# Kernel tuning notes

Hardware: AMD Instinct MI355X
Metric: run time of the kernel (lower is better)

Reference implementation:

```python
import jax, jax.numpy as jnp
import numpy as np


def _cdist(x, y):
    # x: (b, n, c), y: (b, m, c) -> (b, n, m) Euclidean distances
    x2 = jnp.sum(x * x, axis=-1, keepdims=True)          # (b, n, 1)
    y2 = jnp.sum(y * y, axis=-1)[:, None, :]             # (b, 1, m)
    xy = jnp.einsum('bnc,bmc->bnm', x, y)                # (b, n, m)
    d2 = jnp.maximum(x2 + y2 - 2.0 * xy, 0.0)
    return jnp.sqrt(d2)


def setup_inputs() -> dict:
    key = jax.random.key(0)
    k1, k2, k3, k4 = jax.random.split(key, 4)
    bs, N, M, C = 8, 4096, 4096, 128
    return {
        'set1': jax.random.normal(k1, (bs, N, C), dtype=jnp.float32),
        'set2': jax.random.normal(k2, (bs, M, C), dtype=jnp.float32),
        'w1': jax.random.uniform(k3, (bs, N), dtype=jnp.float32),
        'w2': jax.random.uniform(k4, (bs, M), dtype=jnp.float32),
    }


def reference(set1, set2, w1, w2):
    dist = _cdist(set1, set2)                 # (b, N, M)
    out_dist = jnp.min(dist, axis=2)          # (b, N)
    out_dist2 = jnp.min(dist, axis=1)         # (b, M)
    total = (jnp.sum(w1 * out_dist) + jnp.sum(w2 * out_dist2)) / 2.0
    return total
```

## Files before the change

### kernel.cpp

```cpp
#include <hip/hip_runtime.h>

#define BS 8
#define NN 4096
#define MM 4096
#define CC 128
#define XT 128
#define MT 128
#define MH 2048
#define NMT (MH / MT)
#define NXT (NN / XT)

#define FINF_BITS 0x7F800000u

typedef __attribute__((ext_vector_type(8))) short bf16x8;
typedef __attribute__((ext_vector_type(4))) float f32x4;

__device__ inline ushort f2bf(float f) {
    unsigned u = __float_as_uint(f);
    unsigned r = (u + 0x7FFFu + ((u >> 16) & 1u)) >> 16;
    return (ushort)r;
}

__global__ void ch_prep(const float* __restrict__ x, const float* __restrict__ y,
                        ushort* __restrict__ x16, ushort* __restrict__ y16,
                        float* __restrict__ xn, float* __restrict__ yn,
                        unsigned* __restrict__ rowmin, unsigned* __restrict__ colmin,
                        float* __restrict__ out) {
    int gid = blockIdx.x * blockDim.x + threadIdx.x;
    size_t i = (size_t)gid * 4;

    float4 v = *(const float4*)(x + i);
    ushort4 o;
    o.x = f2bf(v.x); o.y = f2bf(v.y); o.z = f2bf(v.z); o.w = f2bf(v.w);
    *(ushort4*)(x16 + i) = o;
    float sx = v.x * v.x + v.y * v.y + v.z * v.z + v.w * v.w;

    float4 w = *(const float4*)(y + i);
    ushort4 p;
    p.x = f2bf(w.x); p.y = f2bf(w.y); p.z = f2bf(w.z); p.w = f2bf(w.w);
    *(ushort4*)(y16 + i) = p;
    float sy = w.x * w.x + w.y * w.y + w.z * w.z + w.w * w.w;

#pragma unroll
    for (int mask = 1; mask <= 16; mask <<= 1) {
        sx += __shfl_xor(sx, mask, 64);
        sy += __shfl_xor(sy, mask, 64);
    }
    if ((threadIdx.x & 31) == 0) {
        int row = gid >> 5;
        xn[row] = sx;
        yn[row] = sy;
    }
    if (gid < BS * NN) {
        rowmin[gid] = FINF_BITS;
        colmin[gid] = FINF_BITS;
    }
    if (gid == 0) out[0] = 0.0f;
}

__global__ __launch_bounds__(512) void ch_tile(
    const ushort* __restrict__ X, const ushort* __restrict__ Y,
    const float* __restrict__ xn, const float* __restrict__ yn,
    unsigned* __restrict__ rowmin, unsigned* __restrict__ colmin) {

    __shared__ ushort xs[XT * CC];
    __shared__ unsigned coltile[MH];
    __shared__ unsigned rowtile[XT];

    const int b  = blockIdx.z;
    const int xt = blockIdx.x;
    const int mh = blockIdx.y;
    const int n0 = xt * XT;
    const int m0 = mh * MH;
    const int tid  = threadIdx.x;
    const int wave = tid >> 6;
    const int lane = tid & 63;
    const int lc   = lane & 15;
    const int quad = lane >> 4;
    const int wm = wave >> 2;
    const int wn = wave & 3;

    const ushort* Xb = X + ((size_t)b * NN + n0) * CC;
#pragma unroll
    for (int s = 0; s < 4; ++s) {
        int flat = s * 512 + tid;
        int r = flat >> 4, c = flat & 15;
        int cs = c ^ (r & 7);
        *(bf16x8*)(xs + r * CC + cs * 8) = *(const bf16x8*)(Xb + (size_t)r * CC + c * 8);
    }
    for (int c2 = tid; c2 < MH; c2 += 512) coltile[c2] = FINF_BITS;
    if (tid < XT) rowtile[tid] = FINF_BITS;
    __syncthreads();

    float rm[4][4];
#pragma unroll
    for (int i = 0; i < 4; ++i)
#pragma unroll
        for (int r = 0; r < 4; ++r) rm[i][r] = __builtin_inff();

    const ushort* Yb  = Y + ((size_t)b * MM + m0) * CC;
    const float*  ynb = yn + (size_t)b * MM + m0;
    const float*  xnb = xn + (size_t)b * NN + n0;
    const int xrow = (wm * 64 + lc) * CC;
    const int xsw  = lc & 7;

#pragma unroll 1
    for (int mt = 0; mt < NMT; ++mt) {
        const ushort* Ymt = Yb + (size_t)(mt * MT + wn * 32 + lc) * CC + quad * 8;

        float ynr[2];
#pragma unroll
        for (int j = 0; j < 2; ++j)
            ynr[j] = ynb[mt * MT + wn * 32 + j * 16 + lc];

        f32x4 acc[4][2];
        const f32x4 z = {0.f, 0.f, 0.f, 0.f};
#pragma unroll
        for (int kt = 0; kt < 4; ++kt) {
            bf16x8 af[4], yf[2];
            const int cs = ((kt * 4 + quad) ^ xsw) * 8;
#pragma unroll
            for (int j = 0; j < 2; ++j)
                yf[j] = *(const bf16x8*)(Ymt + (size_t)j * 16 * CC + kt * 32);
#pragma unroll
            for (int i = 0; i < 4; ++i)
                af[i] = *(const bf16x8*)(xs + xrow + i * 16 * CC + cs);
#pragma unroll
            for (int j = 0; j < 2; ++j)
#pragma unroll
                for (int i = 0; i < 4; ++i)
                    acc[i][j] = __builtin_amdgcn_mfma_f32_16x16x32_bf16(
                        af[i], yf[j], (kt == 0) ? z : acc[i][j], 0, 0, 0);
        }

        float cmv[2];
#pragma unroll
        for (int j = 0; j < 2; ++j) cmv[j] = __builtin_inff();

#pragma unroll
        for (int i = 0; i < 4; ++i) {
            float4 t = *(const float4*)(xnb + wm * 64 + i * 16 + quad * 4);
            float xnr[4] = {t.x, t.y, t.z, t.w};
#pragma unroll
            for (int j = 0; j < 2; ++j) {
                f32x4 a = acc[i][j];
#pragma unroll
                for (int r = 0; r < 4; ++r) {
                    float d2 = xnr[r] + fmaf(-2.0f, a[r], ynr[j]);
                    rm[i][r] = fminf(rm[i][r], d2);
                    cmv[j]   = fminf(cmv[j], d2);
                }
            }
        }

#pragma unroll
        for (int mask = 16; mask <= 32; mask <<= 1)
#pragma unroll
            for (int j = 0; j < 2; ++j)
                cmv[j] = fminf(cmv[j], __shfl_xor(cmv[j], mask, 64));
        if (quad == 0) {
#pragma unroll
            for (int j = 0; j < 2; ++j)
                atomicMin(&coltile[mt * MT + wn * 32 + j * 16 + lc],
                          __float_as_uint(fmaxf(cmv[j], 0.0f)));
        }
    }

#pragma unroll
    for (int mask = 1; mask <= 8; mask <<= 1)
#pragma unroll
        for (int i = 0; i < 4; ++i)
#pragma unroll
            for (int r = 0; r < 4; ++r)
                rm[i][r] = fminf(rm[i][r], __shfl_xor(rm[i][r], mask, 64));
    if (lc == 0) {
#pragma unroll
        for (int i = 0; i < 4; ++i)
#pragma unroll
            for (int r = 0; r < 4; ++r)
                atomicMin(&rowtile[wm * 64 + i * 16 + quad * 4 + r],
                          __float_as_uint(fmaxf(rm[i][r], 0.0f)));
    }

    __syncthreads();
    if (tid < XT)
        atomicMin(&rowmin[(size_t)b * NN + n0 + tid], rowtile[tid]);
    for (int c2 = tid; c2 < MH; c2 += 512)
        atomicMin(&colmin[(size_t)b * MM + m0 + c2], coltile[c2]);
}

__global__ void ch_finalize(const unsigned* __restrict__ rowmin,
                            const unsigned* __restrict__ colmin,
                            const float* __restrict__ w1,
                            const float* __restrict__ w2,
                            float* __restrict__ out) {
    int i = blockIdx.x * blockDim.x + threadIdx.x;
    int stride = gridDim.x * blockDim.x;
    float s = 0.f;
    for (int idx = i; idx < BS * NN; idx += stride)
        s += w1[idx] * sqrtf(__uint_as_float(rowmin[idx])) +
             w2[idx] * sqrtf(__uint_as_float(colmin[idx]));
#pragma unroll
    for (int off = 32; off > 0; off >>= 1) s += __shfl_down(s, off, 64);
    __shared__ float ls[4];
    int lane = threadIdx.x & 63, wv = threadIdx.x >> 6;
    if (lane == 0) ls[wv] = s;
    __syncthreads();
    if (threadIdx.x == 0) {
        float t = ls[0] + ls[1] + ls[2] + ls[3];
        atomicAdd(out, 0.5f * t);
    }
}

extern "C" void kernel_launch(void* const* d_in, const int* in_sizes, int n_in,
                              void* d_out, int out_size, void* d_ws, size_t ws_size,
                              hipStream_t stream) {
    const float* set1 = (const float*)d_in[0];
    const float* set2 = (const float*)d_in[1];
    const float* w1   = (const float*)d_in[2];
    const float* w2   = (const float*)d_in[3];
    float* out = (float*)d_out;

    ushort*   x16    = (ushort*)d_ws;
    ushort*   y16    = x16 + (size_t)BS * NN * CC;
    float*    xn     = (float*)(y16 + (size_t)BS * MM * CC);
    float*    yn     = xn + BS * NN;
    unsigned* rowmin = (unsigned*)(yn + BS * MM);
    unsigned* colmin = rowmin + BS * NN;

    ch_prep<<<BS * NN * CC / 4 / 256, 256, 0, stream>>>(
        set1, set2, x16, y16, xn, yn, rowmin, colmin, out);

    dim3 grid(NXT, MM / MH, BS);
    ch_tile<<<grid, 512, 0, stream>>>(x16, y16, xn, yn, rowmin, colmin);

    ch_finalize<<<64, 256, 0, stream>>>(rowmin, colmin, w1, w2, out);
}
```

Before: 154.9 us.

## Give each block full M range, register double-buffer Y, atomics straight to global colmin

Each block now owns a 128-row X tile and sweeps all of M, so row minima are written directly without global atomics. Each wave takes a 16-column Y strip against all 128 X rows (8 MFMA accumulators), with the X norms held in registers. Y fragments are double-buffered in registers across M tiles to hide global load latency. Column minima go through global atomicMin directly rather than a shared-memory column tile. The grid shrinks to 256 blocks (bs-major order), which may reduce occupancy and adds contention on the global column atomics.

```diff
diff --git a/kernel.cpp b/kernel.cpp
--- a/kernel.cpp
+++ b/kernel.cpp
@@ -6,8 +6,7 @@
 #define CC 128
 #define XT 128
 #define MT 128
-#define MH 2048
-#define NMT (MH / MT)
+#define NMT (MM / MT)
 #define NXT (NN / XT)
 
 #define FINF_BITS 0x7F800000u
@@ -24,8 +23,7 @@
 __global__ void ch_prep(const float* __restrict__ x, const float* __restrict__ y,
                         ushort* __restrict__ x16, ushort* __restrict__ y16,
                         float* __restrict__ xn, float* __restrict__ yn,
-                        unsigned* __restrict__ rowmin, unsigned* __restrict__ colmin,
-                        float* __restrict__ out) {
+                        unsigned* __restrict__ colmin, float* __restrict__ out) {
     int gid = blockIdx.x * blockDim.x + threadIdx.x;
     size_t i = (size_t)gid * 4;
 
@@ -51,34 +49,27 @@
         xn[row] = sx;
         yn[row] = sy;
     }
-    if (gid < BS * NN) {
-        rowmin[gid] = FINF_BITS;
-        colmin[gid] = FINF_BITS;
-    }
+    if (gid < BS * MM) colmin[gid] = FINF_BITS;
     if (gid == 0) out[0] = 0.0f;
 }
 
 __global__ __launch_bounds__(512) void ch_tile(
     const ushort* __restrict__ X, const ushort* __restrict__ Y,
     const float* __restrict__ xn, const float* __restrict__ yn,
-    unsigned* __restrict__ rowmin, unsigned* __restrict__ colmin) {
+    float* __restrict__ rowmin, unsigned* __restrict__ colmin) {
 
     __shared__ ushort xs[XT * CC];
-    __shared__ unsigned coltile[MH];
     __shared__ unsigned rowtile[XT];
 
-    const int b  = blockIdx.z;
-    const int xt = blockIdx.x;
-    const int mh = blockIdx.y;
+    const int b  = blockIdx.x;
+    const int xt = blockIdx.y;
     const int n0 = xt * XT;
-    const int m0 = mh * MH;
     const int tid  = threadIdx.x;
     const int wave = tid >> 6;
     const int lane = tid & 63;
     const int lc   = lane & 15;
     const int quad = lane >> 4;
-    const int wm = wave >> 2;
-    const int wn = wave & 3;
+    const int ycol = wave * 16 + lc;
 
     const ushort* Xb = X + ((size_t)b * NN + n0) * CC;
 #pragma unroll
@@ -88,108 +79,96 @@
         int cs = c ^ (r & 7);
         *(bf16x8*)(xs + r * CC + cs * 8) = *(const bf16x8*)(Xb + (size_t)r * CC + c * 8);
     }
-    for (int c2 = tid; c2 < MH; c2 += 512) coltile[c2] = FINF_BITS;
     if (tid < XT) rowtile[tid] = FINF_BITS;
     __syncthreads();
 
-    float rm[4][4];
-#pragma unroll
-    for (int i = 0; i < 4; ++i)
+    float xnr[8][4];
+#pragma unroll
+    for (int i = 0; i < 8; ++i) {
+        float4 t = *(const float4*)(xn + (size_t)b * NN + n0 + i * 16 + quad * 4);
+        xnr[i][0] = t.x; xnr[i][1] = t.y; xnr[i][2] = t.z; xnr[i][3] = t.w;
+    }
+    float rm[8][4];
+#pragma unroll
+    for (int i = 0; i < 8; ++i)
 #pragma unroll
         for (int r = 0; r < 4; ++r) rm[i][r] = __builtin_inff();
 
-    const ushort* Yb  = Y + ((size_t)b * MM + m0) * CC;
-    const float*  ynb = yn + (size_t)b * MM + m0;
-    const float*  xnb = xn + (size_t)b * NN + n0;
-    const int xrow = (wm * 64 + lc) * CC;
-    const int xsw  = lc & 7;
-
-#pragma unroll 1
-    for (int mt = 0; mt < NMT; ++mt) {
-        const ushort* Ymt = Yb + (size_t)(mt * MT + wn * 32 + lc) * CC + quad * 8;
-
-        float ynr[2];
-#pragma unroll
-        for (int j = 0; j < 2; ++j)
-            ynr[j] = ynb[mt * MT + wn * 32 + j * 16 + lc];
-
-        f32x4 acc[4][2];
+    const ushort* Yb  = Y + (size_t)b * MM * CC;
+    const float*  ynb = yn + (size_t)b * MM;
+    const int xsw = lc & 7;
+
+    auto loady = [&](int mt, bf16x8* yf, float& ynr) {
+        const ushort* yp = Yb + (size_t)(mt * MT + ycol) * CC + quad * 8;
+#pragma unroll
+        for (int kt = 0; kt < 4; ++kt)
+            yf[kt] = *(const bf16x8*)(yp + kt * 32);
+        ynr = ynb[mt * MT + ycol];
+    };
+
+    auto compute = [&](int mt, const bf16x8* yf, float ynr) {
+        f32x4 acc[8];
         const f32x4 z = {0.f, 0.f, 0.f, 0.f};
 #pragma unroll
         for (int kt = 0; kt < 4; ++kt) {
-            bf16x8 af[4], yf[2];
             const int cs = ((kt * 4 + quad) ^ xsw) * 8;
 #pragma unroll
-            for (int j = 0; j < 2; ++j)
-                yf[j] = *(const bf16x8*)(Ymt + (size_t)j * 16 * CC + kt * 32);
-#pragma unroll
-            for (int i = 0; i < 4; ++i)
-                af[i] = *(const bf16x8*)(xs + xrow + i * 16 * CC + cs);
-#pragma unroll
-            for (int j = 0; j < 2; ++j)
-#pragma unroll
-                for (int i = 0; i < 4; ++i)
-                    acc[i][j] = __builtin_amdgcn_mfma_f32_16x16x32_bf16(
-                        af[i], yf[j], (kt == 0) ? z : acc[i][j], 0, 0, 0);
-        }
-
-        float cmv[2];
-#pragma unroll
-        for (int j = 0; j < 2; ++j) cmv[j] = __builtin_inff();
-
-#pragma unroll
-        for (int i = 0; i < 4; ++i) {
-            float4 t = *(const float4*)(xnb + wm * 64 + i * 16 + quad * 4);
-            float xnr[4] = {t.x, t.y, t.z, t.w};
-#pragma unroll
-            for (int j = 0; j < 2; ++j) {
-                f32x4 a = acc[i][j];
-#pragma unroll
-                for (int r = 0; r < 4; ++r) {
-                    float d2 = xnr[r] + fmaf(-2.0f, a[r], ynr[j]);
-                    rm[i][r] = fminf(rm[i][r], d2);
-                    cmv[j]   = fminf(cmv[j], d2);
-                }
+            for (int i = 0; i < 8; ++i) {
+                bf16x8 af = *(const bf16x8*)(xs + (i * 16 + lc) * CC + cs);
+                acc[i] = __builtin_amdgcn_mfma_f32_16x16x32_bf16(
+                    af, yf[kt], (kt == 0) ? z : acc[i], 0, 0, 0);
             }
         }
-
-#pragma unroll
-        for (int mask = 16; mask <= 32; mask <<= 1)
-#pragma unroll
-            for (int j = 0; j < 2; ++j)
-                cmv[j] = fminf(cmv[j], __shfl_xor(cmv[j], mask, 64));
-        if (quad == 0) {
-#pragma unroll
-            for (int j = 0; j < 2; ++j)
-                atomicMin(&coltile[mt * MT + wn * 32 + j * 16 + lc],
-                          __float_as_uint(fmaxf(cmv[j], 0.0f)));
+        float cmv = __builtin_inff();
+#pragma unroll
+        for (int i = 0; i < 8; ++i) {
+            f32x4 a = acc[i];
+#pragma unroll
+            for (int r = 0; r < 4; ++r) {
+                float d2 = xnr[i][r] + fmaf(-2.0f, a[r], ynr);
+                rm[i][r] = fminf(rm[i][r], d2);
+                cmv      = fminf(cmv, d2);
+            }
         }
+        cmv = fminf(cmv, __shfl_xor(cmv, 16, 64));
+        cmv = fminf(cmv, __shfl_xor(cmv, 32, 64));
+        if (quad == 0)
+            atomicMin(&colmin[(size_t)b * MM + mt * MT + ycol],
+                      __float_as_uint(fmaxf(cmv, 0.0f)));
+    };
+
+    bf16x8 yfA[4], yfB[4];
+    float ynrA, ynrB;
+    loady(0, yfA, ynrA);
+#pragma unroll 1
+    for (int mt = 0; mt < NMT; mt += 2) {
+        loady(mt + 1, yfB, ynrB);
+        compute(mt, yfA, ynrA);
+        loady((mt + 2 < NMT) ? mt + 2 : 0, yfA, ynrA);
+        compute(mt + 1, yfB, ynrB);
     }
 
 #pragma unroll
     for (int mask = 1; mask <= 8; mask <<= 1)
 #pragma unroll
-        for (int i = 0; i < 4; ++i)
+        for (int i = 0; i < 8; ++i)
 #pragma unroll
             for (int r = 0; r < 4; ++r)
                 rm[i][r] = fminf(rm[i][r], __shfl_xor(rm[i][r], mask, 64));
     if (lc == 0) {
 #pragma unroll
-        for (int i = 0; i < 4; ++i)
+        for (int i = 0; i < 8; ++i)
 #pragma unroll
             for (int r = 0; r < 4; ++r)
-                atomicMin(&rowtile[wm * 64 + i * 16 + quad * 4 + r],
+                atomicMin(&rowtile[i * 16 + quad * 4 + r],
                           __float_as_uint(fmaxf(rm[i][r], 0.0f)));
     }
-
     __syncthreads();
     if (tid < XT)
-        atomicMin(&rowmin[(size_t)b * NN + n0 + tid], rowtile[tid]);
-    for (int c2 = tid; c2 < MH; c2 += 512)
-        atomicMin(&colmin[(size_t)b * MM + m0 + c2], coltile[c2]);
-}
-
-__global__ void ch_finalize(const unsigned* __restrict__ rowmin,
+        rowmin[(size_t)b * NN + n0 + tid] = __uint_as_float(rowtile[tid]);
+}
+
+__global__ void ch_finalize(const float* __restrict__ rowmin,
                             const unsigned* __restrict__ colmin,
                             const float* __restrict__ w1,
                             const float* __restrict__ w2,
@@ -198,7 +177,7 @@
     int stride = gridDim.x * blockDim.x;
     float s = 0.f;
     for (int idx = i; idx < BS * NN; idx += stride)
-        s += w1[idx] * sqrtf(__uint_as_float(rowmin[idx])) +
+        s += w1[idx] * sqrtf(rowmin[idx]) +
              w2[idx] * sqrtf(__uint_as_float(colmin[idx]));
 #pragma unroll
     for (int off = 32; off > 0; off >>= 1) s += __shfl_down(s, off, 64);
@@ -225,13 +204,13 @@
     ushort*   y16    = x16 + (size_t)BS * NN * CC;
     float*    xn     = (float*)(y16 + (size_t)BS * MM * CC);
     float*    yn     = xn + BS * NN;
-    unsigned* rowmin = (unsigned*)(yn + BS * MM);
-    unsigned* colmin = rowmin + BS * NN;
+    float*    rowmin = yn + BS * MM;
+    unsigned* colmin = (unsigned*)(rowmin + BS * NN);
 
     ch_prep<<<BS * NN * CC / 4 / 256, 256, 0, stream>>>(
-        set1, set2, x16, y16, xn, yn, rowmin, colmin, out);
-
-    dim3 grid(NXT, MM / MH, BS);
+        set1, set2, x16, y16, xn, yn, colmin, out);
+
+    dim3 grid(BS, NXT);
     ch_tile<<<grid, 512, 0, stream>>>(x16, y16, xn, yn, rowmin, colmin);
 
     ch_finalize<<<64, 256, 0, stream>>>(rowmin, colmin, w1, w2, out);
```

Result: slower. 224.4 us (+44.9%).

## Fuse X conversion into tile kernel and fold finalize via last-block reduction

Applied to the files above, without the earlier changes.

The X-side bf16 conversion and row norms move out of the prep kernel and into the tile kernel, which now reads fp32 X directly, converts it while staging into shared memory, and computes the norms there. The separate finalize kernel is removed: a global done counter lets the last tile block do the weighted reduction and write the output. This drops one launch and a round trip through global memory for X16/xn. In exchange, the fp32 X tile is read twice across the M halves, each block does extra conversion work, and a threadfence plus atomic is added per block.

```diff
diff --git a/kernel.cpp b/kernel.cpp
--- a/kernel.cpp
+++ b/kernel.cpp
@@ -9,6 +9,7 @@
 #define MH 2048
 #define NMT (MH / MT)
 #define NXT (NN / XT)
+#define NBLK (NXT * (MM / MH) * BS)
 
 #define FINF_BITS 0x7F800000u
 
@@ -21,19 +22,12 @@
     return (ushort)r;
 }
 
-__global__ void ch_prep(const float* __restrict__ x, const float* __restrict__ y,
-                        ushort* __restrict__ x16, ushort* __restrict__ y16,
-                        float* __restrict__ xn, float* __restrict__ yn,
+__global__ void ch_prep(const float* __restrict__ y,
+                        ushort* __restrict__ y16, float* __restrict__ yn,
                         unsigned* __restrict__ rowmin, unsigned* __restrict__ colmin,
-                        float* __restrict__ out) {
+                        unsigned* __restrict__ done, float* __restrict__ out) {
     int gid = blockIdx.x * blockDim.x + threadIdx.x;
     size_t i = (size_t)gid * 4;
-
-    float4 v = *(const float4*)(x + i);
-    ushort4 o;
-    o.x = f2bf(v.x); o.y = f2bf(v.y); o.z = f2bf(v.z); o.w = f2bf(v.w);
-    *(ushort4*)(x16 + i) = o;
-    float sx = v.x * v.x + v.y * v.y + v.z * v.z + v.w * v.w;
 
     float4 w = *(const float4*)(y + i);
     ushort4 p;
@@ -42,30 +36,27 @@
     float sy = w.x * w.x + w.y * w.y + w.z * w.z + w.w * w.w;
 
 #pragma unroll
-    for (int mask = 1; mask <= 16; mask <<= 1) {
-        sx += __shfl_xor(sx, mask, 64);
+    for (int mask = 1; mask <= 16; mask <<= 1)
         sy += __shfl_xor(sy, mask, 64);
-    }
-    if ((threadIdx.x & 31) == 0) {
-        int row = gid >> 5;
-        xn[row] = sx;
-        yn[row] = sy;
-    }
-    if (gid < BS * NN) {
-        rowmin[gid] = FINF_BITS;
-        colmin[gid] = FINF_BITS;
-    }
-    if (gid == 0) out[0] = 0.0f;
+    if ((threadIdx.x & 31) == 0)
+        yn[gid >> 5] = sy;
+
+    if (gid < BS * NN) rowmin[gid] = FINF_BITS;
+    if (gid < BS * MM) colmin[gid] = FINF_BITS;
+    if (gid == 0) { *done = 0u; out[0] = 0.0f; }
 }
 
 __global__ __launch_bounds__(512) void ch_tile(
-    const ushort* __restrict__ X, const ushort* __restrict__ Y,
-    const float* __restrict__ xn, const float* __restrict__ yn,
-    unsigned* __restrict__ rowmin, unsigned* __restrict__ colmin) {
+    const float* __restrict__ Xf, const ushort* __restrict__ Y,
+    const float* __restrict__ yn,
+    unsigned* __restrict__ rowmin, unsigned* __restrict__ colmin,
+    const float* __restrict__ w1, const float* __restrict__ w2,
+    unsigned* __restrict__ done, float* __restrict__ out) {
 
     __shared__ ushort xs[XT * CC];
     __shared__ unsigned coltile[MH];
     __shared__ unsigned rowtile[XT];
+    __shared__ float xnorm[XT];
 
     const int b  = blockIdx.z;
     const int xt = blockIdx.x;
@@ -80,18 +71,42 @@
     const int wm = wave >> 2;
     const int wn = wave & 3;
 
-    const ushort* Xb = X + ((size_t)b * NN + n0) * CC;
-#pragma unroll
-    for (int s = 0; s < 4; ++s) {
-        int flat = s * 512 + tid;
-        int r = flat >> 4, c = flat & 15;
-        int cs = c ^ (r & 7);
-        *(bf16x8*)(xs + r * CC + cs * 8) = *(const bf16x8*)(Xb + (size_t)r * CC + c * 8);
+    const float* Xb = Xf + ((size_t)b * NN + n0) * CC;
+    {
+        float psum[4];
+#pragma unroll
+        for (int s = 0; s < 4; ++s) {
+            int flat = s * 512 + tid;
+            int r = flat >> 4, c = flat & 15;
+            float4 v0 = *(const float4*)(Xb + (size_t)r * CC + c * 8);
+            float4 v1 = *(const float4*)(Xb + (size_t)r * CC + c * 8 + 4);
+            ushort h[8] = {f2bf(v0.x), f2bf(v0.y), f2bf(v0.z), f2bf(v0.w),
+                           f2bf(v1.x), f2bf(v1.y), f2bf(v1.z), f2bf(v1.w)};
+            *(bf16x8*)(xs + r * CC + (c ^ (r & 7)) * 8) = *(bf16x8*)h;
+            psum[s] = v0.x * v0.x + v0.y * v0.y + v0.z * v0.z + v0.w * v0.w +
+                      v1.x * v1.x + v1.y * v1.y + v1.z * v1.z + v1.w * v1.w;
+        }
+#pragma unroll
+        for (int mask = 1; mask <= 8; mask <<= 1)
+#pragma unroll
+            for (int s = 0; s < 4; ++s)
+                psum[s] += __shfl_xor(psum[s], mask, 64);
+        if ((tid & 15) == 0) {
+#pragma unroll
+            for (int s = 0; s < 4; ++s)
+                xnorm[s * 32 + (tid >> 4)] = psum[s];
+        }
     }
     for (int c2 = tid; c2 < MH; c2 += 512) coltile[c2] = FINF_BITS;
     if (tid < XT) rowtile[tid] = FINF_BITS;
     __syncthreads();
 
+    float xnr[4][4];
+#pragma unroll
+    for (int i = 0; i < 4; ++i) {
+        float4 t = *(const float4*)(&xnorm[wm * 64 + i * 16 + quad * 4]);
+        xnr[i][0] = t.x; xnr[i][1] = t.y; xnr[i][2] = t.z; xnr[i][3] = t.w;
+    }
     float rm[4][4];
 #pragma unroll
     for (int i = 0; i < 4; ++i)
@@ -100,7 +115,6 @@
 
     const ushort* Yb  = Y + ((size_t)b * MM + m0) * CC;
     const float*  ynb = yn + (size_t)b * MM + m0;
-    const float*  xnb = xn + (size_t)b * NN + n0;
     const int xrow = (wm * 64 + lc) * CC;
     const int xsw  = lc & 7;
 
@@ -139,14 +153,12 @@
 
 #pragma unroll
         for (int i = 0; i < 4; ++i) {
-            float4 t = *(const float4*)(xnb + wm * 64 + i * 16 + quad * 4);
-            float xnr[4] = {t.x, t.y, t.z, t.w};
 #pragma unroll
             for (int j = 0; j < 2; ++j) {
                 f32x4 a = acc[i][j];
 #pragma unroll
                 for (int r = 0; r < 4; ++r) {
-                    float d2 = xnr[r] + fmaf(-2.0f, a[r], ynr[j]);
+                    float d2 = xnr[i][r] + fmaf(-2.0f, a[r], ynr[j]);
                     rm[i][r] = fminf(rm[i][r], d2);
                     cmv[j]   = fminf(cmv[j], d2);
                 }
@@ -187,28 +199,29 @@
         atomicMin(&rowmin[(size_t)b * NN + n0 + tid], rowtile[tid]);
     for (int c2 = tid; c2 < MH; c2 += 512)
         atomicMin(&colmin[(size_t)b * MM + m0 + c2], coltile[c2]);
-}
-
-__global__ void ch_finalize(const unsigned* __restrict__ rowmin,
-                            const unsigned* __restrict__ colmin,
-                            const float* __restrict__ w1,
-                            const float* __restrict__ w2,
-                            float* __restrict__ out) {
-    int i = blockIdx.x * blockDim.x + threadIdx.x;
-    int stride = gridDim.x * blockDim.x;
-    float s = 0.f;
-    for (int idx = i; idx < BS * NN; idx += stride)
-        s += w1[idx] * sqrtf(__uint_as_float(rowmin[idx])) +
-             w2[idx] * sqrtf(__uint_as_float(colmin[idx]));
-#pragma unroll
-    for (int off = 32; off > 0; off >>= 1) s += __shfl_down(s, off, 64);
-    __shared__ float ls[4];
-    int lane = threadIdx.x & 63, wv = threadIdx.x >> 6;
-    if (lane == 0) ls[wv] = s;
-    __syncthreads();
-    if (threadIdx.x == 0) {
-        float t = ls[0] + ls[1] + ls[2] + ls[3];
-        atomicAdd(out, 0.5f * t);
+
+    __threadfence();
+    __syncthreads();
+    __shared__ unsigned isLast;
+    if (tid == 0) isLast = (atomicAdd(done, 1u) == NBLK - 1) ? 1u : 0u;
+    __syncthreads();
+    if (isLast) {
+        __threadfence();
+        float s = 0.f;
+        for (int idx = tid; idx < BS * NN; idx += 512)
+            s += w1[idx] * sqrtf(__uint_as_float(rowmin[idx])) +
+                 w2[idx] * sqrtf(__uint_as_float(colmin[idx]));
+#pragma unroll
+        for (int off = 32; off > 0; off >>= 1) s += __shfl_down(s, off, 64);
+        __shared__ float ls[8];
+        if (lane == 0) ls[wave] = s;
+        __syncthreads();
+        if (tid == 0) {
+            float t = 0.f;
+#pragma unroll
+            for (int k = 0; k < 8; ++k) t += ls[k];
+            out[0] = 0.5f * t;
+        }
     }
 }
 
@@ -221,18 +234,16 @@
     const float* w2   = (const float*)d_in[3];
     float* out = (float*)d_out;
 
-    ushort*   x16    = (ushort*)d_ws;
-    ushort*   y16    = x16 + (size_t)BS * NN * CC;
-    float*    xn     = (float*)(y16 + (size_t)BS * MM * CC);
-    float*    yn     = xn + BS * NN;
+    ushort*   y16    = (ushort*)d_ws;
+    float*    yn     = (float*)(y16 + (size_t)BS * MM * CC);
     unsigned* rowmin = (unsigned*)(yn + BS * MM);
     unsigned* colmin = rowmin + BS * NN;
-
-    ch_prep<<<BS * NN * CC / 4 / 256, 256, 0, stream>>>(
-        set1, set2, x16, y16, xn, yn, rowmin, colmin, out);
+    unsigned* done   = colmin + BS * MM;
+
+    ch_prep<<<BS * MM * CC / 4 / 256, 256, 0, stream>>>(
+        set2, y16, yn, rowmin, colmin, done, out);
 
     dim3 grid(NXT, MM / MH, BS);
-    ch_tile<<<grid, 512, 0, stream>>>(x16, y16, xn, yn, rowmin, colmin);
-
-    ch_finalize<<<64, 256, 0, stream>>>(rowmin, colmin, w1, w2, out);
-}
+    ch_tile<<<grid, 512, 0, stream>>>(set1, y16, yn, rowmin, colmin,
+                                      w1, w2, done, out);
+}
```

Result: slower. 230.4 us (+48.7%).
